# Optimization experiments

Hardware: AMD Instinct MI355X
Metric: run time of the kernel (lower is better)

Reference implementation:

```python
import jax, jax.numpy as jnp
import numpy as np
from jax import lax

EPS = 1e-08


def setup_inputs() -> dict:
    key = jax.random.key(0)
    k1, k2, k3, k4 = jax.random.split(key, 4)
    b, cin, cout, hw, kk = 32, 256, 256, 64, 3
    fan_in = cin * kk * kk
    # kaiming_normal_(a=0, mode='fan_in', nonlinearity='leaky_relu') -> gain=sqrt(2), std=sqrt(2/fan_in)
    w_std = np.sqrt(2.0 / fan_in).astype(np.float32)
    return {
        "x": jax.random.normal(k1, (b, cin, hw, hw), dtype=jnp.float32),
        "y": jax.random.normal(k2, (b, cin), dtype=jnp.float32),
        "weight": jax.random.normal(k3, (cout, cin, kk, kk), dtype=jnp.float32) * w_std,
        "bias": jax.random.normal(k4, (cout,), dtype=jnp.float32) * 0.1,
    }


def _modulated_conv(x, y, weight, bias):
    # x: [b, cin, h, w]; y: [b, cin]; weight: [cout, cin, kh, kw]; bias: [cout]
    # modulate: per-sample scale of input channels
    w = weight[None] * (y[:, None, :, None, None] + 1.0)  # [b, cout, cin, kh, kw]
    # demodulate: normalize each (sample, out-channel) filter
    d = lax.rsqrt(jnp.sum(w * w, axis=(2, 3, 4), keepdims=True) + EPS)
    w = w * d

    def conv_one(xi, wi):
        # xi: [cin, h, w]; wi: [cout, cin, kh, kw]
        out = lax.conv_general_dilated(
            xi[None], wi, window_strides=(1, 1), padding="SAME",
            dimension_numbers=("NCHW", "OIHW", "NCHW"))
        return out[0]  # [cout, h, w]

    out = jax.vmap(conv_one)(x, w)  # [b, cout, h, w]
    return out + bias[None, :, None, None]


def reference(x, y, weight, bias):
    return _modulated_conv(x, y, weight, bias)
```

## Files before the change

### kernel.cpp

```cpp
#include <hip/hip_runtime.h>
#include <hip/hip_bf16.h>

typedef __attribute__((ext_vector_type(8))) short short8;
typedef __attribute__((ext_vector_type(4))) float f32x4;

#define XT_IMG_BYTES (66*66*256*2)
#define XT_TOTAL_BYTES (32LL*XT_IMG_BYTES)
#define WM_ROW_BYTES (2304*2)
#define WM_IMG_BYTES (256*WM_ROW_BYTES)

static __device__ __forceinline__ void async16(void* lds, const void* g) {
  __builtin_amdgcn_global_load_lds((const __attribute__((address_space(1))) void*)g,
                                   (__attribute__((address_space(3))) void*)lds, 16, 0, 0);
}
static __device__ __forceinline__ ushort f2bf(float f) {
  __hip_bfloat16 h = __float2bfloat16(f);
  return *reinterpret_cast<ushort*>(&h);
}

__global__ __launch_bounds__(256) void k_prep(const float* __restrict__ x,
                                              const float* __restrict__ W,
                                              const float* __restrict__ y,
                                              ushort* __restrict__ xT,
                                              ushort* __restrict__ wmod) {
  __shared__ float smem[64][65];
  const int bid = blockIdx.x;
  const int t   = threadIdx.x;

  if (bid < 8192) {
    const int b  = bid >> 8;
    const int h  = (bid >> 2) & 63;
    const int c0 = (bid & 3) << 6;
    const int tw = t & 63, tg = t >> 6;
    const float* xp = x + (size_t)(b * 256 + c0) * 4096 + h * 64 + tw;
#pragma unroll
    for (int j = 0; j < 16; ++j) {
      int il = j * 4 + tg;
      smem[il][tw] = xp[(size_t)il * 4096];
    }
    __syncthreads();
    const int q  = t & 7;
    const int w0 = t >> 3;
    ushort* op = xT + (size_t)b * (66 * 66 * 256) + ((size_t)(h + 1) * 66 + 1) * 256 + c0;
#pragma unroll
    for (int j = 0; j < 2; ++j) {
      const int wl = j * 32 + w0;
      short8 v;
#pragma unroll
      for (int k2 = 0; k2 < 8; ++k2) v[k2] = (short)f2bf(smem[8 * q + k2][wl]);
      *(short8*)(op + (size_t)wl * 256 + 8 * q) = v;
    }
  } else if (bid < 16384) {
    float* red = &smem[0][0];
    const int bb = bid - 8192;
    const int b = bb >> 8, o = bb & 255;
    const float* wp = W + (size_t)(o * 256 + t) * 9;
    float wr[9];
#pragma unroll
    for (int r = 0; r < 9; ++r) wr[r] = wp[r];
    const float ym = y[b * 256 + t] + 1.0f;
    float ss = 0.f;
#pragma unroll
    for (int r = 0; r < 9; ++r) ss += wr[r] * wr[r];
    red[t] = ss * ym * ym;
    __syncthreads();
    for (int s = 128; s > 0; s >>= 1) {
      if (t < s) red[t] += red[t + s];
      __syncthreads();
    }
    const float sc = rsqrtf(red[0] + 1e-8f) * ym;
    ushort* op = wmod + (size_t)(b * 256 + o) * 2304 + t;
#pragma unroll
    for (int r = 0; r < 9; ++r) op[r * 256] = f2bf(wr[r] * sc);
  } else {
    const int zb = bid - 16384;
    const int b  = zb >> 3;
    const int tt = ((zb & 7) << 8) | t;
    uint4* xT4 = (uint4*)xT;
    const uint4 z = make_uint4(0u, 0u, 0u, 0u);
    uint4* base = xT4 + (size_t)b * (66 * 66 * 32);
    uint4* r0  = base;
    uint4* r65 = base + (size_t)65 * 66 * 32;
    for (int i = tt; i < 2112; i += 2048) { r0[i] = z; r65[i] = z; }
    {
      int r = (tt >> 5) + 1, c = tt & 31;
      base[((size_t)r * 66 + 0)  * 32 + c] = z;
      base[((size_t)r * 66 + 65) * 32 + c] = z;
    }
  }
}

__global__ __launch_bounds__(512, 2) void k_gemm(const ushort* __restrict__ wmod,
                                                 const ushort* __restrict__ xT,
                                                 const float* __restrict__ bias,
                                                 float* __restrict__ out) {
  __shared__ ushort ldsA[2][16384];
  __shared__ ushort ldsB[2][16384];

  const int t  = threadIdx.x;
  const int bx = blockIdx.x;
  const int xcd = bx & 7;
  const int idx = bx >> 3;
  const int b   = xcd + ((idx >> 4) << 3);
  const int tn  = idx & 15;
  const int n0  = tn << 8;
  const int h0  = tn << 2;

  const int ln = t & 15;
  const int kq = (t >> 4) & 3;
  const int wv = t >> 6;
  const int wm = wv >> 2;
  const int wn = wv & 3;

  const char* wmodB = (const char*)wmod + (size_t)b * WM_IMG_BYTES;
  const char* xTB   = (const char*)xT   + (size_t)b * XT_IMG_BYTES;

  int gAoff[4], gBoff[4];
#pragma unroll
  for (int j = 0; j < 4; ++j) {
    const int s = j * 512 + t;
    const int row = s >> 3, g = s & 7;
    gAoff[j] = row * WM_ROW_BYTES + ((g ^ (row & 7)) << 4);
    const int hr = row >> 6, wc = row & 63;
    gBoff[j] = ((h0 + hr) * 66 + wc) * 512 + ((g ^ (row & 7)) << 4);
  }

  const int swz = ln & 7;
  const int g0 = ((0 | kq) ^ swz) << 3;
  const int g1 = ((4 | kq) ^ swz) << 3;
  const int aBase = (wm * 128 + ln) * 64;
  const int bBase = (wn * 64  + ln) * 64;

  f32x4 acc[8][4];
  const f32x4 z4 = {0.f, 0.f, 0.f, 0.f};
#pragma unroll
  for (int i = 0; i < 8; ++i)
#pragma unroll
    for (int j = 0; j < 4; ++j) acc[i][j] = z4;

#define LOAD_A(J, KO, BUF) async16(&ldsA[BUF][0] + ((J) * 512 + t) * 8, wmodB + gAoff[J] + (KO))
#define LOAD_B(J, KO, BUF) async16(&ldsB[BUF][0] + ((J) * 512 + t) * 8, xTB   + gBoff[J] + (KO))

#define MF(F, E, A, B) acc[F][E] = __builtin_amdgcn_mfma_f32_16x16x32_bf16(A, B, acc[F][E], 0, 0, 0)
#define FENCE() __builtin_amdgcn_sched_barrier(0)
#define BAR()   __builtin_amdgcn_s_barrier()

  LOAD_A(0, 0, 0); LOAD_A(1, 0, 0); LOAD_A(2, 0, 0); LOAD_A(3, 0, 0);
  LOAD_B(0, 0, 0); LOAD_B(1, 0, 0); LOAD_B(2, 0, 0); LOAD_B(3, 0, 0);
  {
    const int koA1 = 0 * 512 + 128;
    const int koB1 = (0 * 66 + 0) * 512 + 128;
    LOAD_A(0, koA1, 1); LOAD_A(2, koA1, 1);
    LOAD_B(0, koB1, 1); LOAD_B(1, koB1, 1); LOAD_B(2, koB1, 1); LOAD_B(3, koB1, 1);
  }
  asm volatile("s_waitcnt vmcnt(6)" ::: "memory");
  FENCE(); BAR(); FENCE();

#pragma unroll 1
  for (int kt = 0; kt < 36; ++kt) {
    const int cur = kt & 1, nb = cur ^ 1;
    const ushort* bufA = &ldsA[cur][0];
    const ushort* bufB = &ldsB[cur][0];

    const int n1 = kt + 1;
    const int koA1 = (n1 >> 2) * 512 + ((n1 & 3) << 7);
    const int n2 = kt + 2;
    const int r2 = n2 >> 2;
    const int kh2 = r2 / 3, kw2 = r2 - kh2 * 3;
    const int koA2 = r2 * 512 + ((n2 & 3) << 7);
    const int koB2 = (kh2 * 66 + kw2) * 512 + ((n2 & 3) << 7);

    short8 A0 = *(const short8*)(bufA + aBase + 0 * 1024 + g0);
    short8 A1 = *(const short8*)(bufA + aBase + 1 * 1024 + g0);
    short8 A2 = *(const short8*)(bufA + aBase + 2 * 1024 + g0);
    short8 A3 = *(const short8*)(bufA + aBase + 3 * 1024 + g0);
    short8 B0 = *(const short8*)(bufB + bBase + 0 * 1024 + g0);
    short8 B1 = *(const short8*)(bufB + bBase + 1 * 1024 + g0);
    short8 B2 = *(const short8*)(bufB + bBase + 2 * 1024 + g0);
    short8 B3 = *(const short8*)(bufB + bBase + 3 * 1024 + g0);
    if (kt < 35) { LOAD_A(1, koA1, nb); LOAD_A(3, koA1, nb); }
    __builtin_amdgcn_s_setprio(1);
    MF(0,0,A0,B0); MF(1,0,A1,B0); MF(2,0,A2,B0); MF(3,0,A3,B0);
    MF(0,1,A0,B1); MF(1,1,A1,B1); MF(2,1,A2,B1); MF(3,1,A3,B1);
    MF(0,2,A0,B2); MF(1,2,A1,B2); MF(2,2,A2,B2); MF(3,2,A3,B2);
    MF(0,3,A0,B3); MF(1,3,A1,B3); MF(2,3,A2,B3); MF(3,3,A3,B3);
    __builtin_amdgcn_s_setprio(0);

    short8 A4 = *(const short8*)(bufA + aBase + 4 * 1024 + g0);
    short8 A5 = *(const short8*)(bufA + aBase + 5 * 1024 + g0);
    short8 A6 = *(const short8*)(bufA + aBase + 6 * 1024 + g0);
    short8 A7 = *(const short8*)(bufA + aBase + 7 * 1024 + g0);
    __builtin_amdgcn_s_setprio(1);
    MF(4,0,A4,B0); MF(5,0,A5,B0); MF(6,0,A6,B0); MF(7,0,A7,B0);
    MF(4,1,A4,B1); MF(5,1,A5,B1); MF(6,1,A6,B1); MF(7,1,A7,B1);
    MF(4,2,A4,B2); MF(5,2,A5,B2); MF(6,2,A6,B2); MF(7,2,A7,B2);
    MF(4,3,A4,B3); MF(5,3,A5,B3); MF(6,3,A6,B3); MF(7,3,A7,B3);
    __builtin_amdgcn_s_setprio(0);
    FENCE();

    short8 C0 = *(const short8*)(bufA + aBase + 0 * 1024 + g1);
    short8 C1 = *(const short8*)(bufA + aBase + 1 * 1024 + g1);
    short8 C2 = *(const short8*)(bufA + aBase + 2 * 1024 + g1);
    short8 C3 = *(const short8*)(bufA + aBase + 3 * 1024 + g1);
    short8 D0 = *(const short8*)(bufB + bBase + 0 * 1024 + g1);
    short8 D1 = *(const short8*)(bufB + bBase + 1 * 1024 + g1);
    short8 D2 = *(const short8*)(bufB + bBase + 2 * 1024 + g1);
    short8 D3 = *(const short8*)(bufB + bBase + 3 * 1024 + g1);
    __builtin_amdgcn_s_setprio(1);
    MF(0,0,C0,D0); MF(1,0,C1,D0); MF(2,0,C2,D0); MF(3,0,C3,D0);
    MF(0,1,C0,D1); MF(1,1,C1,D1); MF(2,1,C2,D1); MF(3,1,C3,D1);
    MF(0,2,C0,D2); MF(1,2,C1,D2); MF(2,2,C2,D2); MF(3,2,C3,D2);
    MF(0,3,C0,D3); MF(1,3,C1,D3); MF(2,3,C2,D3); MF(3,3,C3,D3);
    __builtin_amdgcn_s_setprio(0);

    FENCE(); BAR(); FENCE();

    short8 C4 = *(const short8*)(bufA + aBase + 4 * 1024 + g1);
    short8 C5 = *(const short8*)(bufA + aBase + 5 * 1024 + g1);
    short8 C6 = *(const short8*)(bufA + aBase + 6 * 1024 + g1);
    short8 C7 = *(const short8*)(bufA + aBase + 7 * 1024 + g1);
    if (kt < 34) {
      LOAD_A(0, koA2, cur); LOAD_A(2, koA2, cur);
      LOAD_B(0, koB2, cur); LOAD_B(1, koB2, cur);
      LOAD_B(2, koB2, cur); LOAD_B(3, koB2, cur);
    }
    __builtin_amdgcn_s_setprio(1);
    MF(4,0,C4,D0); MF(5,0,C5,D0); MF(6,0,C6,D0); MF(7,0,C7,D0);
    MF(4,1,C4,D1); MF(5,1,C5,D1); MF(6,1,C6,D1); MF(7,1,C7,D1);
    MF(4,2,C4,D2); MF(5,2,C5,D2); MF(6,2,C6,D2); MF(7,2,C7,D2);
    MF(4,3,C4,D3); MF(5,3,C5,D3); MF(6,3,C6,D3); MF(7,3,C7,D3);
    __builtin_amdgcn_s_setprio(0);

    if (kt < 34) {
      asm volatile("s_waitcnt vmcnt(6)" ::: "memory");
    } else {
      asm volatile("s_waitcnt vmcnt(0)" ::: "memory");
    }
    FENCE(); BAR(); FENCE();
  }

  const float* bp = bias + wm * 128;
  float* outB = out + ((size_t)(b * 256 + wm * 128)) * 4096 + n0 + wn * 64 + ln;
#pragma unroll
  for (int mi = 0; mi < 8; ++mi) {
#pragma unroll
    for (int rg = 0; rg < 4; ++rg) {
      const int orow = mi * 16 + kq * 4 + rg;
      const float bv = bp[orow];
      float* po = outB + (size_t)orow * 4096;
#pragma unroll
      for (int ni = 0; ni < 4; ++ni) po[ni * 16] = acc[mi][ni][rg] + bv;
    }
  }
#undef LOAD_A
#undef LOAD_B
#undef MF
#undef FENCE
#undef BAR
}

extern "C" void kernel_launch(void* const* d_in, const int* in_sizes, int n_in,
                              void* d_out, int out_size, void* d_ws, size_t ws_size,
                              hipStream_t stream) {
  const float* x    = (const float*)d_in[0];
  const float* y    = (const float*)d_in[1];
  const float* W    = (const float*)d_in[2];
  const float* bias = (const float*)d_in[3];
  float* out = (float*)d_out;

  ushort* xT   = (ushort*)d_ws;
  ushort* wmod = (ushort*)((char*)d_ws + (size_t)XT_TOTAL_BYTES);

  k_prep<<<16640, 256, 0, stream>>>(x, W, y, xT, wmod);
  k_gemm<<<512,   512, 0, stream>>>(wmod, xT, bias, out);
}
```

Measured before the change: 373.8 us.

## Vectorize x transpose loads, batch weight demod per channel, interleave GEMM LDS reads

The prep kernel now loads x with float4 reads into a padded shared tile. The weight-modulation blocks are reorganized so each block handles one output channel and loops over all 32 samples, using wave shuffles for the reduction, which cuts the prep grid roughly in half. The GEMM main loop is rescheduled with sched_group_barrier hints so LDS reads for the next MFMA group overlap with the current MFMA group, and the trailing fence is dropped. The risks are register pressure from loading the fragments earlier, and less parallelism in the weight prep.

```diff
diff --git a/kernel.cpp b/kernel.cpp
--- a/kernel.cpp
+++ b/kernel.cpp
@@ -23,7 +23,7 @@
                                               const float* __restrict__ y,
                                               ushort* __restrict__ xT,
                                               ushort* __restrict__ wmod) {
-  __shared__ float smem[64][65];
+  __shared__ float smem[64][68];
   const int bid = blockIdx.x;
   const int t   = threadIdx.x;
 
@@ -31,12 +31,12 @@
     const int b  = bid >> 8;
     const int h  = (bid >> 2) & 63;
     const int c0 = (bid & 3) << 6;
-    const int tw = t & 63, tg = t >> 6;
-    const float* xp = x + (size_t)(b * 256 + c0) * 4096 + h * 64 + tw;
-#pragma unroll
-    for (int j = 0; j < 16; ++j) {
-      int il = j * 4 + tg;
-      smem[il][tw] = xp[(size_t)il * 4096];
+    const float* xp = x + (size_t)(b * 256 + c0) * 4096 + h * 64;
+#pragma unroll
+    for (int j = 0; j < 4; ++j) {
+      const int lin = j * 1024 + t * 4;
+      const int il = lin >> 6, c = lin & 63;
+      *(float4*)&smem[il][c] = *(const float4*)(xp + (size_t)il * 4096 + c);
     }
     __syncthreads();
     const int q  = t & 7;
@@ -50,30 +50,34 @@
       for (int k2 = 0; k2 < 8; ++k2) v[k2] = (short)f2bf(smem[8 * q + k2][wl]);
       *(short8*)(op + (size_t)wl * 256 + 8 * q) = v;
     }
-  } else if (bid < 16384) {
+  } else if (bid < 8448) {
     float* red = &smem[0][0];
-    const int bb = bid - 8192;
-    const int b = bb >> 8, o = bb & 255;
+    const int o = bid - 8192;
     const float* wp = W + (size_t)(o * 256 + t) * 9;
     float wr[9];
 #pragma unroll
     for (int r = 0; r < 9; ++r) wr[r] = wp[r];
-    const float ym = y[b * 256 + t] + 1.0f;
     float ss = 0.f;
 #pragma unroll
     for (int r = 0; r < 9; ++r) ss += wr[r] * wr[r];
-    red[t] = ss * ym * ym;
-    __syncthreads();
-    for (int s = 128; s > 0; s >>= 1) {
-      if (t < s) red[t] += red[t + s];
+    const int lane = t & 63, wid = t >> 6;
+#pragma unroll 1
+    for (int b = 0; b < 32; ++b) {
+      const float ym = y[b * 256 + t] + 1.0f;
+      float v = ss * ym * ym;
+#pragma unroll
+      for (int k = 1; k < 64; k <<= 1) v += __shfl_xor(v, k, 64);
+      if (lane == 0) red[wid] = v;
       __syncthreads();
-    }
-    const float sc = rsqrtf(red[0] + 1e-8f) * ym;
-    ushort* op = wmod + (size_t)(b * 256 + o) * 2304 + t;
-#pragma unroll
-    for (int r = 0; r < 9; ++r) op[r * 256] = f2bf(wr[r] * sc);
+      const float tot = red[0] + red[1] + red[2] + red[3];
+      const float sc = rsqrtf(tot + 1e-8f) * ym;
+      ushort* op = wmod + ((size_t)(b * 256 + o)) * 2304 + t;
+#pragma unroll
+      for (int r = 0; r < 9; ++r) op[r * 256] = f2bf(wr[r] * sc);
+      __syncthreads();
+    }
   } else {
-    const int zb = bid - 16384;
+    const int zb = bid - 8448;
     const int b  = zb >> 3;
     const int tt = ((zb & 7) << 8) | t;
     uint4* xT4 = (uint4*)xT;
@@ -144,12 +148,13 @@
 #define MF(F, E, A, B) acc[F][E] = __builtin_amdgcn_mfma_f32_16x16x32_bf16(A, B, acc[F][E], 0, 0, 0)
 #define FENCE() __builtin_amdgcn_sched_barrier(0)
 #define BAR()   __builtin_amdgcn_s_barrier()
+#define SGB(M, N) __builtin_amdgcn_sched_group_barrier((M), (N), 0)
 
   LOAD_A(0, 0, 0); LOAD_A(1, 0, 0); LOAD_A(2, 0, 0); LOAD_A(3, 0, 0);
   LOAD_B(0, 0, 0); LOAD_B(1, 0, 0); LOAD_B(2, 0, 0); LOAD_B(3, 0, 0);
   {
-    const int koA1 = 0 * 512 + 128;
-    const int koB1 = (0 * 66 + 0) * 512 + 128;
+    const int koA1 = 128;
+    const int koB1 = 128;
     LOAD_A(0, koA1, 1); LOAD_A(2, koA1, 1);
     LOAD_B(0, koB1, 1); LOAD_B(1, koB1, 1); LOAD_B(2, koB1, 1); LOAD_B(3, koB1, 1);
   }
@@ -158,9 +163,9 @@
 
 #pragma unroll 1
   for (int kt = 0; kt < 36; ++kt) {
-    const int cur = kt & 1, nb = cur ^ 1;
-    const ushort* bufA = &ldsA[cur][0];
-    const ushort* bufB = &ldsB[cur][0];
+    const int s = kt & 1, sn = s ^ 1;
+    const ushort* bufA = &ldsA[s][0];
+    const ushort* bufB = &ldsB[s][0];
 
     const int n1 = kt + 1;
     const int koA1 = (n1 >> 2) * 512 + ((n1 & 3) << 7);
@@ -178,26 +183,19 @@
     short8 B1 = *(const short8*)(bufB + bBase + 1 * 1024 + g0);
     short8 B2 = *(const short8*)(bufB + bBase + 2 * 1024 + g0);
     short8 B3 = *(const short8*)(bufB + bBase + 3 * 1024 + g0);
-    if (kt < 35) { LOAD_A(1, koA1, nb); LOAD_A(3, koA1, nb); }
+    short8 A4 = *(const short8*)(bufA + aBase + 4 * 1024 + g0);
+    short8 A5 = *(const short8*)(bufA + aBase + 5 * 1024 + g0);
+    short8 A6 = *(const short8*)(bufA + aBase + 6 * 1024 + g0);
+    short8 A7 = *(const short8*)(bufA + aBase + 7 * 1024 + g0);
+    if (kt < 35) { LOAD_A(1, koA1, sn); LOAD_A(3, koA1, sn); }
+    SGB(0x100, 12);
     __builtin_amdgcn_s_setprio(1);
     MF(0,0,A0,B0); MF(1,0,A1,B0); MF(2,0,A2,B0); MF(3,0,A3,B0);
     MF(0,1,A0,B1); MF(1,1,A1,B1); MF(2,1,A2,B1); MF(3,1,A3,B1);
     MF(0,2,A0,B2); MF(1,2,A1,B2); MF(2,2,A2,B2); MF(3,2,A3,B2);
     MF(0,3,A0,B3); MF(1,3,A1,B3); MF(2,3,A2,B3); MF(3,3,A3,B3);
     __builtin_amdgcn_s_setprio(0);
-
-    short8 A4 = *(const short8*)(bufA + aBase + 4 * 1024 + g0);
-    short8 A5 = *(const short8*)(bufA + aBase + 5 * 1024 + g0);
-    short8 A6 = *(const short8*)(bufA + aBase + 6 * 1024 + g0);
-    short8 A7 = *(const short8*)(bufA + aBase + 7 * 1024 + g0);
-    __builtin_amdgcn_s_setprio(1);
-    MF(4,0,A4,B0); MF(5,0,A5,B0); MF(6,0,A6,B0); MF(7,0,A7,B0);
-    MF(4,1,A4,B1); MF(5,1,A5,B1); MF(6,1,A6,B1); MF(7,1,A7,B1);
-    MF(4,2,A4,B2); MF(5,2,A5,B2); MF(6,2,A6,B2); MF(7,2,A7,B2);
-    MF(4,3,A4,B3); MF(5,3,A5,B3); MF(6,3,A6,B3); MF(7,3,A7,B3);
-    __builtin_amdgcn_s_setprio(0);
-    FENCE();
-
+    SGB(0x8, 16);
     short8 C0 = *(const short8*)(bufA + aBase + 0 * 1024 + g1);
     short8 C1 = *(const short8*)(bufA + aBase + 1 * 1024 + g1);
     short8 C2 = *(const short8*)(bufA + aBase + 2 * 1024 + g1);
@@ -206,23 +204,33 @@
     short8 D1 = *(const short8*)(bufB + bBase + 1 * 1024 + g1);
     short8 D2 = *(const short8*)(bufB + bBase + 2 * 1024 + g1);
     short8 D3 = *(const short8*)(bufB + bBase + 3 * 1024 + g1);
+    SGB(0x100, 8);
+    __builtin_amdgcn_s_setprio(1);
+    MF(4,0,A4,B0); MF(5,0,A5,B0); MF(6,0,A6,B0); MF(7,0,A7,B0);
+    MF(4,1,A4,B1); MF(5,1,A5,B1); MF(6,1,A6,B1); MF(7,1,A7,B1);
+    MF(4,2,A4,B2); MF(5,2,A5,B2); MF(6,2,A6,B2); MF(7,2,A7,B2);
+    MF(4,3,A4,B3); MF(5,3,A5,B3); MF(6,3,A6,B3); MF(7,3,A7,B3);
+    __builtin_amdgcn_s_setprio(0);
+    SGB(0x8, 16);
+    short8 C4 = *(const short8*)(bufA + aBase + 4 * 1024 + g1);
+    short8 C5 = *(const short8*)(bufA + aBase + 5 * 1024 + g1);
+    short8 C6 = *(const short8*)(bufA + aBase + 6 * 1024 + g1);
+    short8 C7 = *(const short8*)(bufA + aBase + 7 * 1024 + g1);
+    SGB(0x100, 4);
     __builtin_amdgcn_s_setprio(1);
     MF(0,0,C0,D0); MF(1,0,C1,D0); MF(2,0,C2,D0); MF(3,0,C3,D0);
     MF(0,1,C0,D1); MF(1,1,C1,D1); MF(2,1,C2,D1); MF(3,1,C3,D1);
     MF(0,2,C0,D2); MF(1,2,C1,D2); MF(2,2,C2,D2); MF(3,2,C3,D2);
     MF(0,3,C0,D3); MF(1,3,C1,D3); MF(2,3,C2,D3); MF(3,3,C3,D3);
     __builtin_amdgcn_s_setprio(0);
+    SGB(0x8, 16);
 
     FENCE(); BAR(); FENCE();
 
-    short8 C4 = *(const short8*)(bufA + aBase + 4 * 1024 + g1);
-    short8 C5 = *(const short8*)(bufA + aBase + 5 * 1024 + g1);
-    short8 C6 = *(const short8*)(bufA + aBase + 6 * 1024 + g1);
-    short8 C7 = *(const short8*)(bufA + aBase + 7 * 1024 + g1);
     if (kt < 34) {
-      LOAD_A(0, koA2, cur); LOAD_A(2, koA2, cur);
-      LOAD_B(0, koB2, cur); LOAD_B(1, koB2, cur);
-      LOAD_B(2, koB2, cur); LOAD_B(3, koB2, cur);
+      LOAD_A(0, koA2, s); LOAD_A(2, koA2, s);
+      LOAD_B(0, koB2, s); LOAD_B(1, koB2, s);
+      LOAD_B(2, koB2, s); LOAD_B(3, koB2, s);
     }
     __builtin_amdgcn_s_setprio(1);
     MF(4,0,C4,D0); MF(5,0,C5,D0); MF(6,0,C6,D0); MF(7,0,C7,D0);
@@ -236,7 +244,7 @@
     } else {
       asm volatile("s_waitcnt vmcnt(0)" ::: "memory");
     }
-    FENCE(); BAR(); FENCE();
+    FENCE(); BAR();
   }
 
   const float* bp = bias + wm * 128;
@@ -257,6 +265,7 @@
 #undef MF
 #undef FENCE
 #undef BAR
+#undef SGB
 }
 
 extern "C" void kernel_launch(void* const* d_in, const int* in_sizes, int n_in,
@@ -271,6 +280,6 @@
   ushort* xT   = (ushort*)d_ws;
   ushort* wmod = (ushort*)((char*)d_ws + (size_t)XT_TOTAL_BYTES);
 
-  k_prep<<<16640, 256, 0, stream>>>(x, W, y, xT, wmod);
-  k_gemm<<<512,   512, 0, stream>>>(wmod, xT, bias, out);
-}
+  k_prep<<<8704, 256, 0, stream>>>(x, W, y, xT, wmod);
+  k_gemm<<<512,  512, 0, stream>>>(wmod, xT, bias, out);
+}
```

Result: slower. 385.2 us (+3.1%).
